# Kernel tuning notes

Hardware: AMD Instinct MI355X
Metric: run time of the kernel (lower is better)

## Reference

```python
import jax, jax.numpy as jnp
import numpy as np

C = 256
R = 16
B, H, W = 16, 128, 128


def _se(d, w1, b1, w2, b2):
    # SE block on [B, C] descriptor: 1x1 convs == linear layers
    h = jax.nn.relu(d @ w1.T + b1)
    return h @ w2.T + b2


def setup_inputs() -> dict:
    key = jax.random.key(0)
    ks = jax.random.split(key, 16)
    s = 0.05
    Cr = C // R
    inp = {
        "x": jax.random.normal(ks[0], (B, C, H, W), jnp.float32),
        # saeb_std
        "w1s": jax.random.normal(ks[1], (Cr, C), jnp.float32) * s,
        "b1s": jnp.zeros((Cr,), jnp.float32),
        "w2s": jax.random.normal(ks[2], (C, Cr), jnp.float32) * s,
        "b2s": jnp.zeros((C,), jnp.float32),
        # saeb_mean
        "w1m": jax.random.normal(ks[3], (Cr, C), jnp.float32) * s,
        "b1m": jnp.zeros((Cr,), jnp.float32),
        "w2m": jax.random.normal(ks[4], (C, Cr), jnp.float32) * s,
        "b2m": jnp.zeros((C,), jnp.float32),
        # bottleneck 2C -> C
        "wb": jax.random.normal(ks[5], (C, 2 * C), jnp.float32) * s,
        "bb": jnp.zeros((C,), jnp.float32),
        # saeb_final
        "w1f": jax.random.normal(ks[6], (Cr, C), jnp.float32) * s,
        "b1f": jnp.zeros((Cr,), jnp.float32),
        "w2f": jax.random.normal(ks[7], (C, Cr), jnp.float32) * s,
        "b2f": jnp.zeros((C,), jnp.float32),
    }
    return inp


def reference(x, w1s, b1s, w2s, b2s, w1m, b1m, w2m, b2m, wb, bb, w1f, b1f, w2f, b2f):
    # Channel descriptors: spatial mean and (biased) std per channel -> [B, C]
    mean = x.mean(axis=(2, 3))
    var = ((x - mean[:, :, None, None]) ** 2).mean(axis=(2, 3))
    std = jnp.sqrt(var)
    ref_std = _se(std, w1s, b1s, w2s, b2s)
    ref_mean = _se(mean, w1m, b1m, w2m, b2m)
    fused = jnp.concatenate([ref_std, ref_mean], axis=1)  # [B, 2C]
    fused = jax.nn.relu(fused @ wb.T + bb)  # [B, C]
    fused = _se(fused, w1f, b1f, w2f, b2f)
    mask = jax.nn.sigmoid(fused)
    return x * mask[:, :, None, None]
```

## Files before the change

kernel.cpp:

```cpp
#include <hip/hip_runtime.h>
#include <math.h>

#define C_ 256
#define CR_ 16
#define B_ 16
#define HW_ (128*128)

typedef float f32x4 __attribute__((ext_vector_type(4)));

__global__ __launch_bounds__(256) void stats_kernel(const float* __restrict__ x,
                                                    float* __restrict__ mean_out,
                                                    float* __restrict__ std_out) {
    const int ch = blockIdx.x;
    const f32x4* xp = (const f32x4*)(x + (size_t)ch * HW_);
    const int t = threadIdx.x;
    float s = 0.f, ss = 0.f;
    #pragma unroll
    for (int i = 0; i < HW_ / 4 / 256; ++i) {
        f32x4 v = xp[t + i * 256];
        s  += v.x + v.y + v.z + v.w;
        ss += v.x * v.x + v.y * v.y + v.z * v.z + v.w * v.w;
    }
    #pragma unroll
    for (int off = 32; off > 0; off >>= 1) {
        s  += __shfl_down(s, off, 64);
        ss += __shfl_down(ss, off, 64);
    }
    __shared__ float ls[4], lss[4];
    const int wid = t >> 6;
    if ((t & 63) == 0) { ls[wid] = s; lss[wid] = ss; }
    __syncthreads();
    if (t == 0) {
        float S  = ls[0] + ls[1] + ls[2] + ls[3];
        float SS = lss[0] + lss[1] + lss[2] + lss[3];
        float m = S * (1.0f / HW_);
        float v = SS * (1.0f / HW_) - m * m;
        mean_out[ch] = m;
        std_out[ch]  = sqrtf(fmaxf(v, 0.f));
    }
}

__global__ __launch_bounds__(256) void mlp_kernel(
    const float* __restrict__ mean_d, const float* __restrict__ std_d,
    const float* __restrict__ w1s, const float* __restrict__ b1s,
    const float* __restrict__ w2s, const float* __restrict__ b2s,
    const float* __restrict__ w1m, const float* __restrict__ b1m,
    const float* __restrict__ w2m, const float* __restrict__ b2m,
    const float* __restrict__ wb,  const float* __restrict__ bb,
    const float* __restrict__ w1f, const float* __restrict__ b1f,
    const float* __restrict__ w2f, const float* __restrict__ b2f,
    float* __restrict__ mask_out)
{
    const int b = blockIdx.x;
    const int t = threadIdx.x;
    __shared__ float ds[C_], dm[C_];
    __shared__ float h1s[CR_], h1m[CR_];
    __shared__ float fused[2 * C_];
    __shared__ float fb[C_];
    __shared__ float h1f[CR_];

    ds[t] = std_d[b * C_ + t];
    dm[t] = mean_d[b * C_ + t];
    __syncthreads();

    if (t < 32) {
        const int r = t & 15;
        const bool is_std = (t < 16);
        const float* w   = is_std ? w1s : w1m;
        const float* src = is_std ? ds : dm;
        float acc = is_std ? b1s[r] : b1m[r];
        for (int c = 0; c < C_; ++c) acc += src[c] * w[r * C_ + c];
        acc = fmaxf(acc, 0.f);
        if (is_std) h1s[r] = acc; else h1m[r] = acc;
    }
    __syncthreads();

    {
        float accs = b2s[t], accm = b2m[t];
        #pragma unroll
        for (int r = 0; r < CR_; ++r) {
            accs += h1s[r] * w2s[t * CR_ + r];
            accm += h1m[r] * w2m[t * CR_ + r];
        }
        fused[t]      = accs;
        fused[C_ + t] = accm;
    }
    __syncthreads();

    {
        float acc = bb[t];
        const f32x4* wr = (const f32x4*)(wb + (size_t)t * 2 * C_);
        #pragma unroll 4
        for (int j = 0; j < 2 * C_ / 4; ++j) {
            f32x4 w4 = wr[j];
            acc += fused[4 * j]     * w4.x + fused[4 * j + 1] * w4.y
                 + fused[4 * j + 2] * w4.z + fused[4 * j + 3] * w4.w;
        }
        fb[t] = fmaxf(acc, 0.f);
    }
    __syncthreads();

    if (t < 16) {
        float acc = b1f[t];
        for (int c = 0; c < C_; ++c) acc += fb[c] * w1f[t * C_ + c];
        h1f[t] = fmaxf(acc, 0.f);
    }
    __syncthreads();

    {
        float acc = b2f[t];
        #pragma unroll
        for (int r = 0; r < CR_; ++r) acc += h1f[r] * w2f[t * CR_ + r];
        mask_out[b * C_ + t] = 1.0f / (1.0f + expf(-acc));
    }
}

__global__ __launch_bounds__(256) void scale_kernel(const float* __restrict__ x,
                                                    const float* __restrict__ mask,
                                                    float* __restrict__ out) {
    const size_t n4 = (size_t)B_ * C_ * HW_ / 4;
    const f32x4* xp = (const f32x4*)x;
    f32x4* op = (f32x4*)out;
    const size_t stride = (size_t)gridDim.x * blockDim.x;
    #pragma unroll 4
    for (size_t i = (size_t)blockIdx.x * blockDim.x + threadIdx.x; i < n4; i += stride) {
        const size_t ch = i >> 12;
        const float m = mask[ch];
        f32x4 v = xp[i];
        v.x *= m; v.y *= m; v.z *= m; v.w *= m;
        __builtin_nontemporal_store(v, op + i);
    }
}

extern "C" void kernel_launch(void* const* d_in, const int* in_sizes, int n_in,
                              void* d_out, int out_size, void* d_ws, size_t ws_size,
                              hipStream_t stream) {
    const float* x   = (const float*)d_in[0];
    const float* w1s = (const float*)d_in[1];
    const float* b1s = (const float*)d_in[2];
    const float* w2s = (const float*)d_in[3];
    const float* b2s = (const float*)d_in[4];
    const float* w1m = (const float*)d_in[5];
    const float* b1m = (const float*)d_in[6];
    const float* w2m = (const float*)d_in[7];
    const float* b2m = (const float*)d_in[8];
    const float* wb  = (const float*)d_in[9];
    const float* bb  = (const float*)d_in[10];
    const float* w1f = (const float*)d_in[11];
    const float* b1f = (const float*)d_in[12];
    const float* w2f = (const float*)d_in[13];
    const float* b2f = (const float*)d_in[14];
    float* out = (float*)d_out;

    float* mean_ws = (float*)d_ws;
    float* std_ws  = mean_ws + B_ * C_;
    float* mask_ws = std_ws + B_ * C_;

    stats_kernel<<<B_ * C_, 256, 0, stream>>>(x, mean_ws, std_ws);
    mlp_kernel<<<B_, 256, 0, stream>>>(mean_ws, std_ws,
                                       w1s, b1s, w2s, b2s,
                                       w1m, b1m, w2m, b2m,
                                       wb, bb, w1f, b1f, w2f, b2f,
                                       mask_ws);
    scale_kernel<<<2048, 256, 0, stream>>>(x, mask_ws, out);
}
```

Before: 159.8 us.

## Fuse stats, MLP and scale into one cooperative kernel with grid barriers

```diff
diff --git a/kernel.cpp b/kernel.cpp
--- a/kernel.cpp
+++ b/kernel.cpp
@@ -6,42 +6,40 @@
 #define B_ 16
 #define HW_ (128*128)
 
+#define NBLK 256
+#define TPB  512
+#define CPB  16
+#define CPW  2
+#define CD   16
+
 typedef float f32x4 __attribute__((ext_vector_type(4)));
 
-__global__ __launch_bounds__(256) void stats_kernel(const float* __restrict__ x,
-                                                    float* __restrict__ mean_out,
-                                                    float* __restrict__ std_out) {
-    const int ch = blockIdx.x;
-    const f32x4* xp = (const f32x4*)(x + (size_t)ch * HW_);
-    const int t = threadIdx.x;
-    float s = 0.f, ss = 0.f;
-    #pragma unroll
-    for (int i = 0; i < HW_ / 4 / 256; ++i) {
-        f32x4 v = xp[t + i * 256];
-        s  += v.x + v.y + v.z + v.w;
-        ss += v.x * v.x + v.y * v.y + v.z * v.z + v.w * v.w;
-    }
-    #pragma unroll
-    for (int off = 32; off > 0; off >>= 1) {
-        s  += __shfl_down(s, off, 64);
-        ss += __shfl_down(ss, off, 64);
-    }
-    __shared__ float ls[4], lss[4];
-    const int wid = t >> 6;
-    if ((t & 63) == 0) { ls[wid] = s; lss[wid] = ss; }
+__device__ __forceinline__ float agent_load(const float* p) {
+    return __hip_atomic_load(p, __ATOMIC_RELAXED, __HIP_MEMORY_SCOPE_AGENT);
+}
+__device__ __forceinline__ void agent_store(float* p, float v) {
+    __hip_atomic_store(p, v, __ATOMIC_RELAXED, __HIP_MEMORY_SCOPE_AGENT);
+}
+
+__device__ __forceinline__ void grid_barrier(unsigned* cnt, unsigned* gen) {
     __syncthreads();
-    if (t == 0) {
-        float S  = ls[0] + ls[1] + ls[2] + ls[3];
-        float SS = lss[0] + lss[1] + lss[2] + lss[3];
-        float m = S * (1.0f / HW_);
-        float v = SS * (1.0f / HW_) - m * m;
-        mean_out[ch] = m;
-        std_out[ch]  = sqrtf(fmaxf(v, 0.f));
-    }
-}
-
-__global__ __launch_bounds__(256) void mlp_kernel(
-    const float* __restrict__ mean_d, const float* __restrict__ std_d,
+    if (threadIdx.x == 0) {
+        unsigned old = __hip_atomic_fetch_add(cnt, 1u, __ATOMIC_ACQ_REL,
+                                              __HIP_MEMORY_SCOPE_AGENT);
+        if (old == (unsigned)(NBLK - 1)) {
+            __hip_atomic_store(gen, 1u, __ATOMIC_RELEASE, __HIP_MEMORY_SCOPE_AGENT);
+        } else {
+            while (__hip_atomic_load(gen, __ATOMIC_ACQUIRE,
+                                     __HIP_MEMORY_SCOPE_AGENT) == 0u) {
+                __builtin_amdgcn_s_sleep(2);
+            }
+        }
+    }
+    __syncthreads();
+}
+
+__global__ __launch_bounds__(TPB, 2) void fused_kernel(
+    const float* __restrict__ x,
     const float* __restrict__ w1s, const float* __restrict__ b1s,
     const float* __restrict__ w2s, const float* __restrict__ b2s,
     const float* __restrict__ w1m, const float* __restrict__ b1m,
@@ -49,86 +47,135 @@
     const float* __restrict__ wb,  const float* __restrict__ bb,
     const float* __restrict__ w1f, const float* __restrict__ b1f,
     const float* __restrict__ w2f, const float* __restrict__ b2f,
-    float* __restrict__ mask_out)
+    float* __restrict__ out,
+    float* mean_ws, float* std_ws, float* mask_ws, unsigned* bar)
 {
-    const int b = blockIdx.x;
-    const int t = threadIdx.x;
+    const int bid  = blockIdx.x;
+    const int t    = threadIdx.x;
+    const int w    = t >> 6;
+    const int lane = t & 63;
+
     __shared__ float ds[C_], dm[C_];
     __shared__ float h1s[CR_], h1m[CR_];
     __shared__ float fused[2 * C_];
     __shared__ float fb[C_];
     __shared__ float h1f[CR_];
 
-    ds[t] = std_d[b * C_ + t];
-    dm[t] = mean_d[b * C_ + t];
-    __syncthreads();
-
-    if (t < 32) {
-        const int r = t & 15;
-        const bool is_std = (t < 16);
-        const float* w   = is_std ? w1s : w1m;
-        const float* src = is_std ? ds : dm;
-        float acc = is_std ? b1s[r] : b1m[r];
-        for (int c = 0; c < C_; ++c) acc += src[c] * w[r * C_ + c];
-        acc = fmaxf(acc, 0.f);
-        if (is_std) h1s[r] = acc; else h1m[r] = acc;
-    }
-    __syncthreads();
-
-    {
-        float accs = b2s[t], accm = b2m[t];
+    f32x4 cache[CPW][CD];
+
+    #pragma unroll
+    for (int cc = 0; cc < CPW; ++cc) {
+        const int gch = bid * CPB + w * CPW + cc;
+        const f32x4* xp = (const f32x4*)(x + (size_t)gch * HW_);
+        float s = 0.f, ss = 0.f;
         #pragma unroll
-        for (int r = 0; r < CR_; ++r) {
-            accs += h1s[r] * w2s[t * CR_ + r];
-            accm += h1m[r] * w2m[t * CR_ + r];
-        }
-        fused[t]      = accs;
-        fused[C_ + t] = accm;
-    }
-    __syncthreads();
-
-    {
-        float acc = bb[t];
-        const f32x4* wr = (const f32x4*)(wb + (size_t)t * 2 * C_);
+        for (int i = 0; i < CD; ++i) {
+            f32x4 v = xp[lane + i * 64];
+            cache[cc][i] = v;
+            s  += v.x + v.y + v.z + v.w;
+            ss += v.x * v.x + v.y * v.y + v.z * v.z + v.w * v.w;
+        }
         #pragma unroll 4
-        for (int j = 0; j < 2 * C_ / 4; ++j) {
-            f32x4 w4 = wr[j];
-            acc += fused[4 * j]     * w4.x + fused[4 * j + 1] * w4.y
-                 + fused[4 * j + 2] * w4.z + fused[4 * j + 3] * w4.w;
-        }
-        fb[t] = fmaxf(acc, 0.f);
-    }
-    __syncthreads();
-
-    if (t < 16) {
-        float acc = b1f[t];
-        for (int c = 0; c < C_; ++c) acc += fb[c] * w1f[t * C_ + c];
-        h1f[t] = fmaxf(acc, 0.f);
-    }
-    __syncthreads();
-
-    {
-        float acc = b2f[t];
+        for (int i = CD; i < 64; ++i) {
+            f32x4 v = xp[lane + i * 64];
+            s  += v.x + v.y + v.z + v.w;
+            ss += v.x * v.x + v.y * v.y + v.z * v.z + v.w * v.w;
+        }
         #pragma unroll
-        for (int r = 0; r < CR_; ++r) acc += h1f[r] * w2f[t * CR_ + r];
-        mask_out[b * C_ + t] = 1.0f / (1.0f + expf(-acc));
-    }
-}
-
-__global__ __launch_bounds__(256) void scale_kernel(const float* __restrict__ x,
-                                                    const float* __restrict__ mask,
-                                                    float* __restrict__ out) {
-    const size_t n4 = (size_t)B_ * C_ * HW_ / 4;
-    const f32x4* xp = (const f32x4*)x;
-    f32x4* op = (f32x4*)out;
-    const size_t stride = (size_t)gridDim.x * blockDim.x;
-    #pragma unroll 4
-    for (size_t i = (size_t)blockIdx.x * blockDim.x + threadIdx.x; i < n4; i += stride) {
-        const size_t ch = i >> 12;
-        const float m = mask[ch];
-        f32x4 v = xp[i];
-        v.x *= m; v.y *= m; v.z *= m; v.w *= m;
-        __builtin_nontemporal_store(v, op + i);
+        for (int m = 1; m < 64; m <<= 1) {
+            s  += __shfl_xor(s, m, 64);
+            ss += __shfl_xor(ss, m, 64);
+        }
+        if (lane == 0) {
+            float mean = s * (1.0f / HW_);
+            float var  = ss * (1.0f / HW_) - mean * mean;
+            agent_store(&mean_ws[gch], mean);
+            agent_store(&std_ws[gch], sqrtf(fmaxf(var, 0.f)));
+        }
+    }
+
+    grid_barrier(&bar[0], &bar[1]);
+
+    if (bid < B_) {
+        const int b = bid;
+        if (t < C_) {
+            ds[t] = agent_load(&std_ws[b * C_ + t]);
+            dm[t] = agent_load(&mean_ws[b * C_ + t]);
+        }
+        __syncthreads();
+
+        if (t < 32) {
+            const int r = t & 15;
+            const bool is_std = (t < 16);
+            const float* wgt = is_std ? w1s : w1m;
+            const float* src = is_std ? ds : dm;
+            float acc = is_std ? b1s[r] : b1m[r];
+            for (int c = 0; c < C_; ++c) acc += src[c] * wgt[r * C_ + c];
+            acc = fmaxf(acc, 0.f);
+            if (is_std) h1s[r] = acc; else h1m[r] = acc;
+        }
+        __syncthreads();
+
+        if (t < C_) {
+            float accs = b2s[t], accm = b2m[t];
+            #pragma unroll
+            for (int r = 0; r < CR_; ++r) {
+                accs += h1s[r] * w2s[t * CR_ + r];
+                accm += h1m[r] * w2m[t * CR_ + r];
+            }
+            fused[t]      = accs;
+            fused[C_ + t] = accm;
+        }
+        __syncthreads();
+
+        if (t < C_) {
+            float acc = bb[t];
+            const f32x4* wr = (const f32x4*)(wb + (size_t)t * 2 * C_);
+            #pragma unroll 4
+            for (int j = 0; j < 2 * C_ / 4; ++j) {
+                f32x4 w4 = wr[j];
+                acc += fused[4 * j]     * w4.x + fused[4 * j + 1] * w4.y
+                     + fused[4 * j + 2] * w4.z + fused[4 * j + 3] * w4.w;
+            }
+            fb[t] = fmaxf(acc, 0.f);
+        }
+        __syncthreads();
+
+        if (t < CR_) {
+            float acc = b1f[t];
+            for (int c = 0; c < C_; ++c) acc += fb[c] * w1f[t * C_ + c];
+            h1f[t] = fmaxf(acc, 0.f);
+        }
+        __syncthreads();
+
+        if (t < C_) {
+            float acc = b2f[t];
+            #pragma unroll
+            for (int r = 0; r < CR_; ++r) acc += h1f[r] * w2f[t * CR_ + r];
+            agent_store(&mask_ws[b * C_ + t], 1.0f / (1.0f + expf(-acc)));
+        }
+    }
+
+    grid_barrier(&bar[2], &bar[3]);
+
+    #pragma unroll
+    for (int cc = 0; cc < CPW; ++cc) {
+        const int gch = bid * CPB + w * CPW + cc;
+        const float m = agent_load(&mask_ws[gch]);
+        const f32x4* xp = (const f32x4*)(x + (size_t)gch * HW_);
+        f32x4* op = (f32x4*)(out + (size_t)gch * HW_);
+        #pragma unroll
+        for (int i = 0; i < CD; ++i) {
+            f32x4 v = cache[cc][i];
+            v.x *= m; v.y *= m; v.z *= m; v.w *= m;
+            __builtin_nontemporal_store(v, op + lane + i * 64);
+        }
+        #pragma unroll 4
+        for (int i = CD; i < 64; ++i) {
+            f32x4 v = xp[lane + i * 64];
+            v.x *= m; v.y *= m; v.z *= m; v.w *= m;
+            __builtin_nontemporal_store(v, op + lane + i * 64);
+        }
     }
 }
 
@@ -152,15 +199,27 @@
     const float* b2f = (const float*)d_in[14];
     float* out = (float*)d_out;
 
-    float* mean_ws = (float*)d_ws;
-    float* std_ws  = mean_ws + B_ * C_;
-    float* mask_ws = std_ws + B_ * C_;
-
-    stats_kernel<<<B_ * C_, 256, 0, stream>>>(x, mean_ws, std_ws);
-    mlp_kernel<<<B_, 256, 0, stream>>>(mean_ws, std_ws,
-                                       w1s, b1s, w2s, b2s,
-                                       w1m, b1m, w2m, b2m,
-                                       wb, bb, w1f, b1f, w2f, b2f,
-                                       mask_ws);
-    scale_kernel<<<2048, 256, 0, stream>>>(x, mask_ws, out);
-}
+    float*    mean_ws = (float*)d_ws;
+    float*    std_ws  = mean_ws + B_ * C_;
+    float*    mask_ws = std_ws + B_ * C_;
+    unsigned* bar     = (unsigned*)(mask_ws + B_ * C_);
+
+    hipMemsetAsync((void*)bar, 0, 4 * sizeof(unsigned), stream);
+
+    void* args[] = {
+        (void*)&x,
+        (void*)&w1s, (void*)&b1s, (void*)&w2s, (void*)&b2s,
+        (void*)&w1m, (void*)&b1m, (void*)&w2m, (void*)&b2m,
+        (void*)&wb,  (void*)&bb,
+        (void*)&w1f, (void*)&b1f, (void*)&w2f, (void*)&b2f,
+        (void*)&out,
+        (void*)&mean_ws, (void*)&std_ws, (void*)&mask_ws, (void*)&bar,
+    };
+    hipError_t err = hipLaunchCooperativeKernel((const void*)fused_kernel,
+                                                dim3(NBLK), dim3(TPB), args, 0, stream);
+    if (err != hipSuccess) {
+        fused_kernel<<<dim3(NBLK), dim3(TPB), 0, stream>>>(
+            x, w1s, b1s, w2s, b2s, w1m, b1m, w2m, b2m, wb, bb,
+            w1f, b1f, w2f, b2f, out, mean_ws, std_ws, mask_ws, bar);
+    }
+}
```

Result: slower. 272.0 us (+70.2%).

## Fuse channel stats and SE MLP via last-block atomic counter

Applied to the files above, without the earlier changes.

```diff
diff --git a/kernel.cpp b/kernel.cpp
--- a/kernel.cpp
+++ b/kernel.cpp
@@ -5,15 +5,32 @@
 #define CR_ 16
 #define B_ 16
 #define HW_ (128*128)
+#define NCH (B_ * C_)
 
 typedef float f32x4 __attribute__((ext_vector_type(4)));
 
-__global__ __launch_bounds__(256) void stats_kernel(const float* __restrict__ x,
-                                                    float* __restrict__ mean_out,
-                                                    float* __restrict__ std_out) {
+__device__ __forceinline__ float agent_load(const float* p) {
+    return __hip_atomic_load(p, __ATOMIC_RELAXED, __HIP_MEMORY_SCOPE_AGENT);
+}
+__device__ __forceinline__ void agent_store(float* p, float v) {
+    __hip_atomic_store(p, v, __ATOMIC_RELAXED, __HIP_MEMORY_SCOPE_AGENT);
+}
+
+__global__ __launch_bounds__(256) void stats_mlp_kernel(
+    const float* __restrict__ x,
+    const float* __restrict__ w1s, const float* __restrict__ b1s,
+    const float* __restrict__ w2s, const float* __restrict__ b2s,
+    const float* __restrict__ w1m, const float* __restrict__ b1m,
+    const float* __restrict__ w2m, const float* __restrict__ b2m,
+    const float* __restrict__ wb,  const float* __restrict__ bb,
+    const float* __restrict__ w1f, const float* __restrict__ b1f,
+    const float* __restrict__ w2f, const float* __restrict__ b2f,
+    float* mean_ws, float* std_ws, float* mask_out, unsigned* cnt)
+{
     const int ch = blockIdx.x;
+    const int t  = threadIdx.x;
     const f32x4* xp = (const f32x4*)(x + (size_t)ch * HW_);
-    const int t = threadIdx.x;
+
     float s = 0.f, ss = 0.f;
     #pragma unroll
     for (int i = 0; i < HW_ / 4 / 256; ++i) {
@@ -35,100 +52,98 @@
         float SS = lss[0] + lss[1] + lss[2] + lss[3];
         float m = S * (1.0f / HW_);
         float v = SS * (1.0f / HW_) - m * m;
-        mean_out[ch] = m;
-        std_out[ch]  = sqrtf(fmaxf(v, 0.f));
+        agent_store(&mean_ws[ch], m);
+        agent_store(&std_ws[ch], sqrtf(fmaxf(v, 0.f)));
     }
-}
+    __syncthreads();
 
-__global__ __launch_bounds__(256) void mlp_kernel(
-    const float* __restrict__ mean_d, const float* __restrict__ std_d,
-    const float* __restrict__ w1s, const float* __restrict__ b1s,
-    const float* __restrict__ w2s, const float* __restrict__ b2s,
-    const float* __restrict__ w1m, const float* __restrict__ b1m,
-    const float* __restrict__ w2m, const float* __restrict__ b2m,
-    const float* __restrict__ wb,  const float* __restrict__ bb,
-    const float* __restrict__ w1f, const float* __restrict__ b1f,
-    const float* __restrict__ w2f, const float* __restrict__ b2f,
-    float* __restrict__ mask_out)
-{
-    const int b = blockIdx.x;
-    const int t = threadIdx.x;
+    __shared__ unsigned is_last;
+    if (t == 0) {
+        unsigned old = __hip_atomic_fetch_add(cnt, 1u, __ATOMIC_ACQ_REL,
+                                              __HIP_MEMORY_SCOPE_AGENT);
+        is_last = (old == (unsigned)(NCH - 1));
+    }
+    __syncthreads();
+    if (!is_last) return;
+
     __shared__ float ds[C_], dm[C_];
     __shared__ float h1s[CR_], h1m[CR_];
-    __shared__ float fused[2 * C_];
+    __shared__ float fsd[2 * C_];
     __shared__ float fb[C_];
     __shared__ float h1f[CR_];
 
-    ds[t] = std_d[b * C_ + t];
-    dm[t] = mean_d[b * C_ + t];
-    __syncthreads();
+    for (int b = 0; b < B_; ++b) {
+        ds[t] = agent_load(&std_ws[b * C_ + t]);
+        dm[t] = agent_load(&mean_ws[b * C_ + t]);
+        __syncthreads();
 
-    if (t < 32) {
-        const int r = t & 15;
-        const bool is_std = (t < 16);
-        const float* w   = is_std ? w1s : w1m;
-        const float* src = is_std ? ds : dm;
-        float acc = is_std ? b1s[r] : b1m[r];
-        for (int c = 0; c < C_; ++c) acc += src[c] * w[r * C_ + c];
-        acc = fmaxf(acc, 0.f);
-        if (is_std) h1s[r] = acc; else h1m[r] = acc;
-    }
-    __syncthreads();
+        if (t < 32) {
+            const int r = t & 15;
+            const bool is_std = (t < 16);
+            const float* wgt = is_std ? w1s : w1m;
+            const float* src = is_std ? ds : dm;
+            float acc = is_std ? b1s[r] : b1m[r];
+            for (int c = 0; c < C_; ++c) acc += src[c] * wgt[r * C_ + c];
+            acc = fmaxf(acc, 0.f);
+            if (is_std) h1s[r] = acc; else h1m[r] = acc;
+        }
+        __syncthreads();
 
-    {
-        float accs = b2s[t], accm = b2m[t];
-        #pragma unroll
-        for (int r = 0; r < CR_; ++r) {
-            accs += h1s[r] * w2s[t * CR_ + r];
-            accm += h1m[r] * w2m[t * CR_ + r];
+        {
+            float accs = b2s[t], accm = b2m[t];
+            #pragma unroll
+            for (int r = 0; r < CR_; ++r) {
+                accs += h1s[r] * w2s[t * CR_ + r];
+                accm += h1m[r] * w2m[t * CR_ + r];
+            }
+            fsd[t]      = accs;
+            fsd[C_ + t] = accm;
         }
-        fused[t]      = accs;
-        fused[C_ + t] = accm;
-    }
-    __syncthreads();
+        __syncthreads();
 
-    {
-        float acc = bb[t];
-        const f32x4* wr = (const f32x4*)(wb + (size_t)t * 2 * C_);
-        #pragma unroll 4
-        for (int j = 0; j < 2 * C_ / 4; ++j) {
-            f32x4 w4 = wr[j];
-            acc += fused[4 * j]     * w4.x + fused[4 * j + 1] * w4.y
-                 + fused[4 * j + 2] * w4.z + fused[4 * j + 3] * w4.w;
+        {
+            float acc = bb[t];
+            const f32x4* wr = (const f32x4*)(wb + (size_t)t * 2 * C_);
+            #pragma unroll 4
+            for (int j = 0; j < 2 * C_ / 4; ++j) {
+                f32x4 w4 = wr[j];
+                acc += fsd[4 * j]     * w4.x + fsd[4 * j + 1] * w4.y
+                     + fsd[4 * j + 2] * w4.z + fsd[4 * j + 3] * w4.w;
+            }
+            fb[t] = fmaxf(acc, 0.f);
         }
-        fb[t] = fmaxf(acc, 0.f);
-    }
-    __syncthreads();
+        __syncthreads();
 
-    if (t < 16) {
-        float acc = b1f[t];
-        for (int c = 0; c < C_; ++c) acc += fb[c] * w1f[t * C_ + c];
-        h1f[t] = fmaxf(acc, 0.f);
-    }
-    __syncthreads();
+        if (t < CR_) {
+            float acc = b1f[t];
+            for (int c = 0; c < C_; ++c) acc += fb[c] * w1f[t * C_ + c];
+            h1f[t] = fmaxf(acc, 0.f);
+        }
+        __syncthreads();
 
-    {
-        float acc = b2f[t];
-        #pragma unroll
-        for (int r = 0; r < CR_; ++r) acc += h1f[r] * w2f[t * CR_ + r];
-        mask_out[b * C_ + t] = 1.0f / (1.0f + expf(-acc));
+        {
+            float acc = b2f[t];
+            #pragma unroll
+            for (int r = 0; r < CR_; ++r) acc += h1f[r] * w2f[t * CR_ + r];
+            mask_out[b * C_ + t] = 1.0f / (1.0f + expf(-acc));
+        }
+        __syncthreads();
     }
 }
 
 __global__ __launch_bounds__(256) void scale_kernel(const float* __restrict__ x,
                                                     const float* __restrict__ mask,
                                                     float* __restrict__ out) {
-    const size_t n4 = (size_t)B_ * C_ * HW_ / 4;
-    const f32x4* xp = (const f32x4*)x;
-    f32x4* op = (f32x4*)out;
-    const size_t stride = (size_t)gridDim.x * blockDim.x;
-    #pragma unroll 4
-    for (size_t i = (size_t)blockIdx.x * blockDim.x + threadIdx.x; i < n4; i += stride) {
-        const size_t ch = i >> 12;
-        const float m = mask[ch];
-        f32x4 v = xp[i];
+    const int ch = blockIdx.x;
+    const int t  = threadIdx.x;
+    const float m = mask[ch];
+    const f32x4* xp = (const f32x4*)(x + (size_t)ch * HW_);
+    f32x4* op = (f32x4*)(out + (size_t)ch * HW_);
+    #pragma unroll
+    for (int i = 0; i < HW_ / 4 / 256; ++i) {
+        f32x4 v = xp[t + i * 256];
         v.x *= m; v.y *= m; v.z *= m; v.w *= m;
-        __builtin_nontemporal_store(v, op + i);
+        __builtin_nontemporal_store(v, op + t + i * 256);
     }
 }
 
@@ -152,15 +167,16 @@
     const float* b2f = (const float*)d_in[14];
     float* out = (float*)d_out;
 
-    float* mean_ws = (float*)d_ws;
-    float* std_ws  = mean_ws + B_ * C_;
-    float* mask_ws = std_ws + B_ * C_;
+    float*    mean_ws = (float*)d_ws;
+    float*    std_ws  = mean_ws + NCH;
+    float*    mask_ws = std_ws + NCH;
+    unsigned* cnt     = (unsigned*)(mask_ws + NCH);
 
-    stats_kernel<<<B_ * C_, 256, 0, stream>>>(x, mean_ws, std_ws);
-    mlp_kernel<<<B_, 256, 0, stream>>>(mean_ws, std_ws,
-                                       w1s, b1s, w2s, b2s,
-                                       w1m, b1m, w2m, b2m,
-                                       wb, bb, w1f, b1f, w2f, b2f,
-                                       mask_ws);
-    scale_kernel<<<2048, 256, 0, stream>>>(x, mask_ws, out);
+    hipMemsetAsync((void*)cnt, 0, sizeof(unsigned), stream);
+
+    stats_mlp_kernel<<<NCH, 256, 0, stream>>>(x,
+        w1s, b1s, w2s, b2s, w1m, b1m, w2m, b2m,
+        wb, bb, w1f, b1f, w2f, b2f,
+        mean_ws, std_ws, mask_ws, cnt);
+    scale_kernel<<<NCH, 256, 0, stream>>>(x, mask_ws, out);
 }
```

Measured after the change: 580.6 us. 3.63x slower.
